# Optimization experiments

Measured on AMD Instinct MI355X. Metric: run time of the kernel, lower is better.

Reference implementation:

```python
import jax, jax.numpy as jnp
import numpy as np
import math

B, S, D, E, H = 8, 384, 768, 768, 12
HD = E // H
MAXL = 512

def _xavier(key, shape):
    fan_in, fan_out = shape[1], shape[0]
    lim = math.sqrt(6.0 / (fan_in + fan_out))
    return jax.random.uniform(key, shape, jnp.float32, -lim, lim)

def setup_inputs() -> dict:
    key = jax.random.key(0)
    ks = jax.random.split(key, 12)
    return {
        "x": jax.random.normal(ks[0], (B, S, D), jnp.float32),
        "mask": jnp.ones((B, S), jnp.int32),
        "segment_ids": jax.random.randint(ks[1], (B, S), 0, 2).astype(jnp.int32),
        "sep_distances": jax.random.normal(ks[2], (B, S), jnp.float32),
        "Wq": _xavier(ks[3], (E, D)), "bq": jnp.zeros((E,), jnp.float32),
        "Wk": _xavier(ks[4], (E, D)), "bk": jnp.zeros((E,), jnp.float32),
        "Wv": _xavier(ks[5], (E, D)), "bv": jnp.zeros((E,), jnp.float32),
        "rel_emb": jax.random.normal(ks[6], (2 * MAXL - 1, D), jnp.float32),
        "Wpk": _xavier(ks[7], (E, D)), "bpk": jnp.zeros((E,), jnp.float32),
        "Wpq": _xavier(ks[8], (E, D)), "bpq": jnp.zeros((E,), jnp.float32),
        "same_bias": jnp.zeros((H,), jnp.float32),
        "cross_bias": jnp.zeros((H,), jnp.float32),
        "sep_scale": jnp.full((H,), 0.25, jnp.float32),
        "sep_decay": jnp.full((H,), 0.35, jnp.float32),
        "Wo": _xavier(ks[9], (D, E)), "bo": jnp.zeros((D,), jnp.float32),
    }

def reference(x, mask, segment_ids, sep_distances, Wq, bq, Wk, bk, Wv, bv,
              rel_emb, Wpk, bpk, Wpq, bpq, same_bias, cross_bias,
              sep_scale, sep_decay, Wo, bo):
    b, s, _ = x.shape
    def shape_heads(t):  # [b,s,E] -> [b,H,s,HD]
        return t.reshape(b, s, H, HD).transpose(0, 2, 1, 3)
    q = shape_heads(x @ Wq.T + bq)
    k = shape_heads(x @ Wk.T + bk)
    v = shape_heads(x @ Wv.T + bv)
    # relative positions i - j, clamped and shifted
    rel_pos = jnp.arange(s)[:, None] - jnp.arange(s)[None, :]
    rel_pos = jnp.clip(rel_pos, -(MAXL - 1), MAXL - 1) + (MAXL - 1)
    rel = rel_emb[rel_pos]                     # [s,s,D]
    pos_k = (rel @ Wpk.T + bpk).reshape(s, s, H, HD)  # [i,j,h,d]
    pos_q = (rel @ Wpq.T + bpq).reshape(s, s, H, HD)
    c2c = jnp.einsum('bhid,bhjd->bhij', q, k)
    c2p = jnp.einsum('bhid,ijhd->bhij', q, pos_k)
    p2c = jnp.einsum('ijhd,bhjd->bhij', pos_q, k)
    logits = (c2c + c2p + p2c) / math.sqrt(HD * 3.0)
    # segment bias
    same = (segment_ids[:, :, None] == segment_ids[:, None, :]).astype(jnp.float32)[:, None]  # [b,1,s,s]
    cross = 1.0 - same
    hb = lambda p: p[None, :, None, None]
    seg_bias = same * hb(same_bias) + cross * hb(cross_bias)
    abs_sep = jnp.abs(sep_distances)
    gap = jnp.abs(abs_sep[:, :, None] - abs_sep[:, None, :])[:, None]  # [b,1,s,s]
    decay = jax.nn.softplus(sep_decay)[None, :, None, None] + 1e-4
    seg_bias = seg_bias + cross * jnp.exp(-gap * decay) * hb(sep_scale)
    logits = logits + seg_bias
    # mask: [b,s] -> [b,1,1,s]
    m = mask[:, None, None, :]
    logits = jnp.where(m == 0, jnp.float32(-9e15), logits)
    attn = jax.nn.softmax(logits, axis=-1)
    vals = jnp.einsum('bhij,bhjd->bhid', attn, v)
    vals = vals.transpose(0, 2, 1, 3).reshape(b, s, E)
    return vals @ Wo.T + bo
```

## Files before the change

kernel.cpp:

```cpp
#include <hip/hip_runtime.h>
#include <math.h>

#define B_  8
#define S_  384
#define H_  12
#define HD_ 64
#define E_  768
#define D_  768

typedef float  floatx4 __attribute__((ext_vector_type(4)));
typedef __bf16 bf16x8  __attribute__((ext_vector_type(8)));
typedef unsigned int ux4 __attribute__((ext_vector_type(4)));

__device__ __forceinline__ unsigned short f2bf(float f) {
    union { float f; unsigned u; } x; x.f = f;
    unsigned r = x.u + 0x7fff + ((x.u >> 16) & 1);
    return (unsigned short)(r >> 16);
}
__device__ __forceinline__ float bf2f(unsigned short u) {
    union { unsigned u; float f; } x; x.u = ((unsigned)u) << 16;
    return x.f;
}
__device__ __forceinline__ bf16x8 gld8(const unsigned short* p) {
    return __builtin_bit_cast(bf16x8, *(const ux4*)p);
}
__device__ __forceinline__ int tadr(int row, int cD) {
    return (row * 8 + (cD ^ (row & 7))) * 8;
}
__device__ __forceinline__ bf16x8 lds8(const unsigned short* base, int row, int cD) {
    return __builtin_bit_cast(bf16x8, *(const ux4*)(base + tadr(row, cD)));
}

__global__ __launch_bounds__(256) void convert_all(
    const float* __restrict__ x,
    const float* __restrict__ Wq, const float* __restrict__ Wk,
    const float* __restrict__ Wv, const float* __restrict__ Wo,
    const float* __restrict__ Wpk, const float* __restrict__ Wpq,
    const float* __restrict__ rel128,
    unsigned short* __restrict__ xb,
    unsigned short* __restrict__ wqb, unsigned short* __restrict__ wkb,
    unsigned short* __restrict__ wvb, unsigned short* __restrict__ wob,
    unsigned short* __restrict__ wpkb, unsigned short* __restrict__ wpqb,
    unsigned short* __restrict__ relb)
{
    const int seg = blockIdx.y;
    const int e = (blockIdx.x * 256 + threadIdx.x) * 4;
    const float* src;
    unsigned short* dst;
    if (seg < 4)       { src = x + (size_t)seg * 589824; dst = xb + (size_t)seg * 589824; }
    else if (seg == 4) { src = Wq;  dst = wqb; }
    else if (seg == 5) { src = Wk;  dst = wkb; }
    else if (seg == 6) { src = Wv;  dst = wvb; }
    else if (seg == 7) { src = Wo;  dst = wob; }
    else if (seg == 8) { src = Wpk; dst = wpkb; }
    else if (seg == 9) { src = Wpq; dst = wpqb; }
    else               { src = rel128; dst = relb; }

    float4 v;
    if (seg == 10 && e >= 767 * 768) v = make_float4(0.f, 0.f, 0.f, 0.f);
    else                             v = *(const float4*)(src + e);
    ushort4 o;
    o.x = f2bf(v.x); o.y = f2bf(v.y); o.z = f2bf(v.z); o.w = f2bf(v.w);
    *(ushort4*)(dst + e) = o;
}

__global__ __launch_bounds__(256) void proj_all(
    const unsigned short* __restrict__ xb, const unsigned short* __restrict__ relb,
    const unsigned short* __restrict__ wq, const unsigned short* __restrict__ wk,
    const unsigned short* __restrict__ wv, const unsigned short* __restrict__ wpk,
    const unsigned short* __restrict__ wpq,
    const float* __restrict__ bq, const float* __restrict__ bk,
    const float* __restrict__ bv, const float* __restrict__ bpk,
    const float* __restrict__ bpq,
    unsigned short* __restrict__ qb, unsigned short* __restrict__ kb,
    unsigned short* __restrict__ vtb, unsigned short* __restrict__ pkb,
    unsigned short* __restrict__ pqb)
{
    const int bid = blockIdx.x;
    int z, mt, nt;
    if (bid < 864) {
        z = bid / 288; const int r = bid - z * 288; mt = r / 6; nt = r - mt * 6;
    } else {
        const int r2 = bid - 864; z = 3 + r2 / 72;
        const int r = r2 % 72; mt = r / 6; nt = r - mt * 6;
    }
    const int m0 = mt * 64, n0 = nt * 128;

    const unsigned short* A = (z < 3) ? xb : relb;
    const unsigned short* W = (z == 0) ? wq : (z == 1) ? wk : (z == 2) ? wv
                            : (z == 3) ? wpk : wpq;
    const float* bias = (z == 0) ? bq : (z == 1) ? bk : (z == 2) ? bv
                      : (z == 3) ? bpk : bpq;
    unsigned short* C = (z == 0) ? qb : (z == 1) ? kb : (z == 2) ? vtb
                      : (z == 3) ? pkb : pqb;

    __shared__ unsigned short As[64 * 64];
    __shared__ unsigned short Ws[128 * 64];

    const int tid  = threadIdx.x;
    const int lane = tid & 63;
    const int wv_  = tid >> 6;
    const int quad = lane >> 4, l16 = lane & 15;

    floatx4 acc[4][2];
#pragma unroll
    for (int i = 0; i < 4; ++i)
#pragma unroll
        for (int j = 0; j < 2; ++j) acc[i][j] = (floatx4){0.f, 0.f, 0.f, 0.f};

    for (int k0 = 0; k0 < 768; k0 += 64) {
        __syncthreads();
#pragma unroll
        for (int r = 0; r < 2; ++r) {
            const int idx = tid + 256 * r;
            const int row = idx >> 3, cL = idx & 7, cD = cL ^ (row & 7);
            __builtin_amdgcn_global_load_lds(
                (__attribute__((address_space(1))) void*)(A + (size_t)(m0 + row) * 768 + k0 + cD * 8),
                (__attribute__((address_space(3))) void*)&As[idx * 8], 16, 0, 0);
        }
#pragma unroll
        for (int r = 0; r < 4; ++r) {
            const int idx = tid + 256 * r;
            const int row = idx >> 3, cL = idx & 7, cD = cL ^ (row & 7);
            __builtin_amdgcn_global_load_lds(
                (__attribute__((address_space(1))) void*)(W + (size_t)(n0 + row) * 768 + k0 + cD * 8),
                (__attribute__((address_space(3))) void*)&Ws[idx * 8], 16, 0, 0);
        }
        __syncthreads();

        bf16x8 a[4][2], b[2][2];
#pragma unroll
        for (int mi = 0; mi < 4; ++mi)
#pragma unroll
            for (int kc = 0; kc < 2; ++kc)
                a[mi][kc] = lds8(As, mi * 16 + l16, kc * 4 + quad);
#pragma unroll
        for (int ni = 0; ni < 2; ++ni)
#pragma unroll
            for (int kc = 0; kc < 2; ++kc)
                b[ni][kc] = lds8(Ws, wv_ * 32 + ni * 16 + l16, kc * 4 + quad);
#pragma unroll
        for (int mi = 0; mi < 4; ++mi)
#pragma unroll
            for (int ni = 0; ni < 2; ++ni)
#pragma unroll
                for (int kc = 0; kc < 2; ++kc)
                    acc[mi][ni] = __builtin_amdgcn_mfma_f32_16x16x32_bf16(
                        a[mi][kc], b[ni][kc], acc[mi][ni], 0, 0, 0);
    }

#pragma unroll
    for (int ni = 0; ni < 2; ++ni) {
        const int n = n0 + wv_ * 32 + ni * 16 + l16;
        const float bn = bias[n];
#pragma unroll
        for (int mi = 0; mi < 4; ++mi) {
            const int mbase = m0 + mi * 16 + quad * 4;
            if (z == 2) {
                const int bb = mbase / S_, s = mbase - bb * S_;
                const int h = n >> 6, hd = n & 63;
                ushort4 o;
                o.x = f2bf(acc[mi][ni][0] + bn);
                o.y = f2bf(acc[mi][ni][1] + bn);
                o.z = f2bf(acc[mi][ni][2] + bn);
                o.w = f2bf(acc[mi][ni][3] + bn);
                *(ushort4*)&C[(((size_t)(bb * H_ + h) << 6) + hd) * S_ + s] = o;
            } else if (z < 2) {
#pragma unroll
                for (int reg = 0; reg < 4; ++reg) {
                    const int m = mbase + reg;
                    const int bb = m / S_, s = m - bb * S_;
                    const int h = n >> 6, hd = n & 63;
                    C[(((size_t)(bb * H_ + h) * S_ + s) << 6) + hd] =
                        f2bf(acc[mi][ni][reg] + bn);
                }
            } else {
#pragma unroll
                for (int reg = 0; reg < 4; ++reg)
                    C[(size_t)(mbase + reg) * 768 + n] = f2bf(acc[mi][ni][reg] + bn);
            }
        }
    }
}

__global__ __launch_bounds__(256) void gemm_out(
    const unsigned short* __restrict__ A, const unsigned short* __restrict__ W,
    const float* __restrict__ bias, float* __restrict__ C)
{
    const int mt = blockIdx.x / 6, nt = blockIdx.x - mt * 6;
    const int m0 = mt * 64, n0 = nt * 128;

    __shared__ unsigned short As[64 * 64];
    __shared__ unsigned short Ws[128 * 64];

    const int tid  = threadIdx.x;
    const int lane = tid & 63;
    const int wv_  = tid >> 6;
    const int quad = lane >> 4, l16 = lane & 15;

    floatx4 acc[4][2];
#pragma unroll
    for (int i = 0; i < 4; ++i)
#pragma unroll
        for (int j = 0; j < 2; ++j) acc[i][j] = (floatx4){0.f, 0.f, 0.f, 0.f};

    for (int k0 = 0; k0 < 768; k0 += 64) {
        __syncthreads();
#pragma unroll
        for (int r = 0; r < 2; ++r) {
            const int idx = tid + 256 * r;
            const int row = idx >> 3, cL = idx & 7, cD = cL ^ (row & 7);
            __builtin_amdgcn_global_load_lds(
                (__attribute__((address_space(1))) void*)(A + (size_t)(m0 + row) * 768 + k0 + cD * 8),
                (__attribute__((address_space(3))) void*)&As[idx * 8], 16, 0, 0);
        }
#pragma unroll
        for (int r = 0; r < 4; ++r) {
            const int idx = tid + 256 * r;
            const int row = idx >> 3, cL = idx & 7, cD = cL ^ (row & 7);
            __builtin_amdgcn_global_load_lds(
                (__attribute__((address_space(1))) void*)(W + (size_t)(n0 + row) * 768 + k0 + cD * 8),
                (__attribute__((address_space(3))) void*)&Ws[idx * 8], 16, 0, 0);
        }
        __syncthreads();

        bf16x8 a[4][2], b[2][2];
#pragma unroll
        for (int mi = 0; mi < 4; ++mi)
#pragma unroll
            for (int kc = 0; kc < 2; ++kc)
                a[mi][kc] = lds8(As, mi * 16 + l16, kc * 4 + quad);
#pragma unroll
        for (int ni = 0; ni < 2; ++ni)
#pragma unroll
            for (int kc = 0; kc < 2; ++kc)
                b[ni][kc] = lds8(Ws, wv_ * 32 + ni * 16 + l16, kc * 4 + quad);
#pragma unroll
        for (int mi = 0; mi < 4; ++mi)
#pragma unroll
            for (int ni = 0; ni < 2; ++ni)
#pragma unroll
                for (int kc = 0; kc < 2; ++kc)
                    acc[mi][ni] = __builtin_amdgcn_mfma_f32_16x16x32_bf16(
                        a[mi][kc], b[ni][kc], acc[mi][ni], 0, 0, 0);
    }

#pragma unroll
    for (int ni = 0; ni < 2; ++ni) {
        const int n = n0 + wv_ * 32 + ni * 16 + l16;
        const float bn = bias[n];
#pragma unroll
        for (int mi = 0; mi < 4; ++mi)
#pragma unroll
            for (int reg = 0; reg < 4; ++reg) {
                const int m = m0 + mi * 16 + quad * 4 + reg;
                C[(size_t)m * 768 + n] = acc[mi][ni][reg] + bn;
            }
    }
}

__global__ __launch_bounds__(256, 4) void attn_mfma(
    const unsigned short* __restrict__ qg, const unsigned short* __restrict__ kg,
    const unsigned short* __restrict__ vtg,
    const unsigned short* __restrict__ pkg, const unsigned short* __restrict__ pqg,
    const int* __restrict__ seg, const float* __restrict__ sep,
    const int* __restrict__ mask,
    const float* __restrict__ same_bias, const float* __restrict__ cross_bias,
    const float* __restrict__ sep_scale, const float* __restrict__ sep_decay,
    unsigned short* __restrict__ part_O, float* __restrict__ part_ml)
{
    __shared__ float CP[64 * 68];

    const int tid  = threadIdx.x;
    const int lane = tid & 63, w = tid >> 6;
    const int l16  = lane & 15, quad = lane >> 4;
    const int ty = tid >> 4, tx = tid & 15;
    const int it = blockIdx.x, h = blockIdx.y;
    const int b  = blockIdx.z / 6, jt = blockIdx.z - 6 * b;
    const int i0 = it * 64, j0 = jt * 64;
    const size_t bh = (size_t)(b * H_ + h);

    const unsigned short* kbase  = kg  + bh * S_ * 64;
    const unsigned short* vtbase = vtg + bh * 64 * S_;
    const int dbase = i0 - j0 + 320;

    bf16x8 qf[2];
#pragma unroll
    for (int ks = 0; ks < 2; ++ks)
        qf[ks] = gld8(qg + (bh * S_ + i0 + 16 * w + l16) * 64 + ks * 32 + quad * 8);

    bf16x8 kf[4][2];
#pragma unroll
    for (int nj = 0; nj < 4; ++nj)
#pragma unroll
        for (int ks = 0; ks < 2; ++ks)
            kf[nj][ks] = gld8(kbase + (size_t)(j0 + 16 * nj + l16) * 64
                              + ks * 32 + quad * 8);

    float ai_r[4]; int si_r[4];
#pragma unroll
    for (int p = 0; p < 4; ++p) {
        const int ii = 4 * ty + p;
        ai_r[p] = fabsf(sep[b * S_ + i0 + ii]);
        si_r[p] = seg[b * S_ + i0 + ii];
    }
    float aj_r[4]; int sj_r[4], mk_r[4];
#pragma unroll
    for (int r = 0; r < 4; ++r) {
        const int jl = 4 * tx + r;
        aj_r[r] = fabsf(sep[b * S_ + j0 + jl]);
        sj_r[r] = seg[b * S_ + j0 + jl];
        mk_r[r] = mask[b * S_ + j0 + jl];
    }

    const float sb  = same_bias[h];
    const float cb  = cross_bias[h];
    const float ssc = sep_scale[h];
    const float sd  = sep_decay[h];
    const float dec = fmaxf(sd, 0.f) + log1pf(__expf(-fabsf(sd))) + 1e-4f;
    const float isc = 0.07216878364870323f;

#pragma unroll
    for (int nj = 0; nj < 4; ++nj) {
        floatx4 acc = (floatx4){0.f, 0.f, 0.f, 0.f};
#pragma unroll
        for (int ks = 0; ks < 2; ++ks)
            acc = __builtin_amdgcn_mfma_f32_16x16x32_bf16(qf[ks], kf[nj][ks], acc, 0, 0, 0);
#pragma unroll
        for (int reg = 0; reg < 4; ++reg) {
            const int ii = 16 * w + quad * 4 + reg;
            CP[ii * 68 + 16 * nj + l16] = acc[reg];
        }
    }

#pragma unroll
    for (int f = 0; f < 5; ++f) {
        const int nd = w + f;
        floatx4 acc = (floatx4){0.f, 0.f, 0.f, 0.f};
#pragma unroll
        for (int ks = 0; ks < 2; ++ks) {
            bf16x8 bf = gld8(pkg + (size_t)(dbase + 16 * nd + l16) * 768
                             + h * 64 + ks * 32 + quad * 8);
            acc = __builtin_amdgcn_mfma_f32_16x16x32_bf16(qf[ks], bf, acc, 0, 0, 0);
        }
        const int ddloc = 16 * nd + l16;
#pragma unroll
        for (int reg = 0; reg < 4; ++reg) {
            const int ii = 16 * w + quad * 4 + reg;
            const int jj = ii - ddloc + 63;
            if (jj >= 0 && jj < 64)
                CP[ii * 68 + jj] += acc[reg];
        }
    }

#pragma unroll
    for (int f = 0; f < 5; ++f) {
        const int nd = w + f;
        bf16x8 pqf[2];
#pragma unroll
        for (int ks = 0; ks < 2; ++ks)
            pqf[ks] = gld8(pqg + (size_t)(dbase + 16 * nd + l16) * 768
                           + h * 64 + ks * 32 + quad * 8);
#pragma unroll
        for (int g = 0; g < 2; ++g) {
            const int nj = (g == 0) ? (3 - f) : (4 - f);
            if (nj < 0 || nj > 3) continue;
            floatx4 acc = (floatx4){0.f, 0.f, 0.f, 0.f};
#pragma unroll
            for (int ks = 0; ks < 2; ++ks)
                acc = __builtin_amdgcn_mfma_f32_16x16x32_bf16(pqf[ks], kf[nj][ks], acc, 0, 0, 0);
            const int jj = 16 * nj + l16;
#pragma unroll
            for (int reg = 0; reg < 4; ++reg) {
                const int ddloc = 16 * nd + quad * 4 + reg;
                const int ii = ddloc + jj - 63;
                if (ii >= 16 * w && ii < 16 * w + 16)
                    CP[ii * 68 + jj] += acc[reg];
            }
        }
    }

    unsigned short* Pp = (unsigned short*)CP;
    float* pml = part_ml + (size_t)(jt * 576 + ((b * H_ + h) * 6 + it)) * 128;
#pragma unroll
    for (int p = 0; p < 4; ++p) {
        const int ii = 4 * ty + p;
        const float aii = ai_r[p];
        const int   sii = si_r[p];
        float lg[4];
        float tmax = -INFINITY;
#pragma unroll
        for (int r = 0; r < 4; ++r) {
            const int jl = 4 * tx + r;
            float xv = CP[ii * 68 + jl] * isc;
            const float gap = fabsf(aii - aj_r[r]);
            const float bias = (sii == sj_r[r]) ? sb
                             : cb + __expf(-gap * dec) * ssc;
            xv += bias;
            if (mk_r[r] == 0) xv = -9.0e15f;
            lg[r] = xv;
            tmax = fmaxf(tmax, xv);
        }
#pragma unroll
        for (int off = 1; off < 16; off <<= 1)
            tmax = fmaxf(tmax, __shfl_xor(tmax, off));
        float rs = 0.f;
        ushort4 pw;
#pragma unroll
        for (int r = 0; r < 4; ++r) {
            const float e = __expf(lg[r] - tmax);
            rs += e;
            ((unsigned short*)&pw)[r] = f2bf(e);
        }
#pragma unroll
        for (int off = 1; off < 16; off <<= 1)
            rs += __shfl_xor(rs, off);
        if (tx == 0) {
            pml[ii]      = tmax;
            pml[64 + ii] = rs;
        }
        *(ushort4*)&Pp[ii * 136 + 4 * tx] = pw;
    }

    bf16x8 pA[2];
#pragma unroll
    for (int ks = 0; ks < 2; ++ks)
        pA[ks] = __builtin_bit_cast(bf16x8,
            *(const ux4*)&Pp[(16 * w + l16) * 136 + ks * 32 + quad * 8]);
    floatx4 O[4];
#pragma unroll
    for (int nd = 0; nd < 4; ++nd) {
        O[nd] = (floatx4){0.f, 0.f, 0.f, 0.f};
#pragma unroll
        for (int ks = 0; ks < 2; ++ks) {
            bf16x8 bf = gld8(vtbase + (size_t)(16 * nd + l16) * S_
                             + j0 + ks * 32 + quad * 8);
            O[nd] = __builtin_amdgcn_mfma_f32_16x16x32_bf16(pA[ks], bf, O[nd], 0, 0, 0);
        }
    }

    unsigned short* pO = part_O + (size_t)(jt * 576 + ((b * H_ + h) * 6 + it)) * 4096;
#pragma unroll
    for (int nd = 0; nd < 4; ++nd) {
        const int d = 16 * nd + l16;
#pragma unroll
        for (int reg = 0; reg < 4; ++reg) {
            const int ii = 16 * w + quad * 4 + reg;
            pO[ii * 64 + d] = f2bf(O[nd][reg]);
        }
    }
}

__global__ __launch_bounds__(256) void merge_attn(
    const unsigned short* __restrict__ part_O, const float* __restrict__ part_ml,
    unsigned short* __restrict__ vals)
{
    const int idx = blockIdx.x;
    const int b  = idx / (H_ * 6);
    const int r  = idx - b * H_ * 6;
    const int h  = r / 6, it = r - h * 6;
    const int tid = threadIdx.x;
    const int ii = tid >> 2, c = (tid & 3) * 16;

    float m[6], l[6];
#pragma unroll
    for (int jc = 0; jc < 6; ++jc) {
        const float* pml = part_ml + (size_t)(jc * 576 + idx) * 128;
        m[jc] = pml[ii];
        l[jc] = pml[64 + ii];
    }
    float M = m[0];
#pragma unroll
    for (int jc = 1; jc < 6; ++jc) M = fmaxf(M, m[jc]);
    float wsum = 0.f, wc[6];
#pragma unroll
    for (int jc = 0; jc < 6; ++jc) {
        wc[jc] = __expf(m[jc] - M);
        wsum += wc[jc] * l[jc];
    }
    const float inv = (wsum > 0.f) ? 1.f / wsum : 0.f;

    float o[16];
#pragma unroll
    for (int e = 0; e < 16; ++e) o[e] = 0.f;
#pragma unroll
    for (int jc = 0; jc < 6; ++jc) {
        const unsigned short* pO = part_O + ((size_t)(jc * 576 + idx)) * 4096
                                 + ii * 64 + c;
        ux4 u0 = *(const ux4*)pO;
        ux4 u1 = *(const ux4*)(pO + 8);
        const unsigned short* us0 = (const unsigned short*)&u0;
        const unsigned short* us1 = (const unsigned short*)&u1;
#pragma unroll
        for (int e = 0; e < 8; ++e) {
            o[e]     += wc[jc] * bf2f(us0[e]);
            o[8 + e] += wc[jc] * bf2f(us1[e]);
        }
    }
    ushort4 w0, w1, w2, w3;
#pragma unroll
    for (int e = 0; e < 4; ++e) {
        ((unsigned short*)&w0)[e] = f2bf(o[e] * inv);
        ((unsigned short*)&w1)[e] = f2bf(o[4 + e] * inv);
        ((unsigned short*)&w2)[e] = f2bf(o[8 + e] * inv);
        ((unsigned short*)&w3)[e] = f2bf(o[12 + e] * inv);
    }
    unsigned short* dst = vals + ((size_t)(b * S_ + it * 64 + ii)) * E_ + h * 64 + c;
    *(ushort4*)(dst)      = w0;
    *(ushort4*)(dst + 4)  = w1;
    *(ushort4*)(dst + 8)  = w2;
    *(ushort4*)(dst + 12) = w3;
}

extern "C" void kernel_launch(void* const* d_in, const int* in_sizes, int n_in,
                              void* d_out, int out_size, void* d_ws, size_t ws_size,
                              hipStream_t stream)
{
    const float* x         = (const float*)d_in[0];
    const int*   mask      = (const int*)d_in[1];
    const int*   seg       = (const int*)d_in[2];
    const float* sep       = (const float*)d_in[3];
    const float* Wq        = (const float*)d_in[4];
    const float* bq        = (const float*)d_in[5];
    const float* Wk        = (const float*)d_in[6];
    const float* bk        = (const float*)d_in[7];
    const float* Wv        = (const float*)d_in[8];
    const float* bv        = (const float*)d_in[9];
    const float* rel_emb   = (const float*)d_in[10];
    const float* Wpk       = (const float*)d_in[11];
    const float* bpk       = (const float*)d_in[12];
    const float* Wpq       = (const float*)d_in[13];
    const float* bpq       = (const float*)d_in[14];
    const float* same_bias = (const float*)d_in[15];
    const float* cross_bias= (const float*)d_in[16];
    const float* sep_scale = (const float*)d_in[17];
    const float* sep_decay = (const float*)d_in[18];
    const float* Wo        = (const float*)d_in[19];
    const float* bo        = (const float*)d_in[20];

    const size_t QKVN = (size_t)B_ * S_ * E_;
    const size_t WN   = (size_t)768 * 768;

    unsigned short* xb    = (unsigned short*)d_ws;
    unsigned short* wqb   = xb   + QKVN;
    unsigned short* wkb   = wqb  + WN;
    unsigned short* wvb   = wkb  + WN;
    unsigned short* wob   = wvb  + WN;
    unsigned short* wpkb  = wob  + WN;
    unsigned short* wpqb  = wpkb + WN;
    unsigned short* relb  = wpqb + WN;
    unsigned short* qb    = relb + WN;
    unsigned short* kb    = qb   + QKVN;
    unsigned short* vtb   = kb   + QKVN;
    unsigned short* pkb   = vtb  + QKVN;
    unsigned short* pqb   = pkb  + WN;
    unsigned short* valsb = pqb  + WN;
    unsigned short* partO = valsb + QKVN;
    float*          partml= (float*)(partO + (size_t)6 * 576 * 4096);

    convert_all<<<dim3(576, 11), 256, 0, stream>>>(
        x, Wq, Wk, Wv, Wo, Wpk, Wpq, rel_emb + (size_t)128 * D_,
        xb, wqb, wkb, wvb, wob, wpkb, wpqb, relb);

    proj_all<<<dim3(1008), 256, 0, stream>>>(
        xb, relb, wqb, wkb, wvb, wpkb, wpqb,
        bq, bk, bv, bpk, bpq, qb, kb, vtb, pkb, pqb);

    attn_mfma<<<dim3(6, 12, 48), 256, 0, stream>>>(
        qb, kb, vtb, pkb, pqb, seg, sep, mask,
        same_bias, cross_bias, sep_scale, sep_decay, partO, partml);

    merge_attn<<<dim3(576), 256, 0, stream>>>(partO, partml, valsb);

    gemm_out<<<dim3(288), 256, 0, stream>>>(valsb, wob, bo, (float*)d_out);
}
```

Measured before the change: 218.6 us.

## Cut attention split-K from six j-chunks to two with online softmax

Each attention block now loops over three 64-wide key tiles with a running max and sum (online softmax), instead of handling a single key tile. This cuts the number of partial outputs per query tile from six to two, and the merge kernel now combines only two partials. The aim is to reduce partial-result write and read traffic and merge work. In exchange the grid is one third the size, there is more serial work per block, and the occupancy hint drops from 4 to 3 blocks per CU, which may hurt latency hiding.

```diff
diff --git a/kernel.cpp b/kernel.cpp
--- a/kernel.cpp
+++ b/kernel.cpp
@@ -259,7 +259,7 @@
     }
 }
 
-__global__ __launch_bounds__(256, 4) void attn_mfma(
+__global__ __launch_bounds__(256, 3) void attn_mfma(
     const unsigned short* __restrict__ qg, const unsigned short* __restrict__ kg,
     const unsigned short* __restrict__ vtg,
     const unsigned short* __restrict__ pkg, const unsigned short* __restrict__ pqg,
@@ -276,26 +276,17 @@
     const int l16  = lane & 15, quad = lane >> 4;
     const int ty = tid >> 4, tx = tid & 15;
     const int it = blockIdx.x, h = blockIdx.y;
-    const int b  = blockIdx.z / 6, jt = blockIdx.z - 6 * b;
-    const int i0 = it * 64, j0 = jt * 64;
+    const int b  = blockIdx.z >> 1, jh = blockIdx.z & 1;
+    const int i0 = it * 64;
     const size_t bh = (size_t)(b * H_ + h);
 
     const unsigned short* kbase  = kg  + bh * S_ * 64;
     const unsigned short* vtbase = vtg + bh * 64 * S_;
-    const int dbase = i0 - j0 + 320;
 
     bf16x8 qf[2];
 #pragma unroll
     for (int ks = 0; ks < 2; ++ks)
         qf[ks] = gld8(qg + (bh * S_ + i0 + 16 * w + l16) * 64 + ks * 32 + quad * 8);
-
-    bf16x8 kf[4][2];
-#pragma unroll
-    for (int nj = 0; nj < 4; ++nj)
-#pragma unroll
-        for (int ks = 0; ks < 2; ++ks)
-            kf[nj][ks] = gld8(kbase + (size_t)(j0 + 16 * nj + l16) * 64
-                              + ks * 32 + quad * 8);
 
     float ai_r[4]; int si_r[4];
 #pragma unroll
@@ -303,14 +294,6 @@
         const int ii = 4 * ty + p;
         ai_r[p] = fabsf(sep[b * S_ + i0 + ii]);
         si_r[p] = seg[b * S_ + i0 + ii];
-    }
-    float aj_r[4]; int sj_r[4], mk_r[4];
-#pragma unroll
-    for (int r = 0; r < 4; ++r) {
-        const int jl = 4 * tx + r;
-        aj_r[r] = fabsf(sep[b * S_ + j0 + jl]);
-        sj_r[r] = seg[b * S_ + j0 + jl];
-        mk_r[r] = mask[b * S_ + j0 + jl];
     }
 
     const float sb  = same_bias[h];
@@ -320,126 +303,163 @@
     const float dec = fmaxf(sd, 0.f) + log1pf(__expf(-fabsf(sd))) + 1e-4f;
     const float isc = 0.07216878364870323f;
 
-#pragma unroll
-    for (int nj = 0; nj < 4; ++nj) {
-        floatx4 acc = (floatx4){0.f, 0.f, 0.f, 0.f};
-#pragma unroll
-        for (int ks = 0; ks < 2; ++ks)
-            acc = __builtin_amdgcn_mfma_f32_16x16x32_bf16(qf[ks], kf[nj][ks], acc, 0, 0, 0);
-#pragma unroll
-        for (int reg = 0; reg < 4; ++reg) {
-            const int ii = 16 * w + quad * 4 + reg;
-            CP[ii * 68 + 16 * nj + l16] = acc[reg];
-        }
-    }
-
-#pragma unroll
-    for (int f = 0; f < 5; ++f) {
-        const int nd = w + f;
-        floatx4 acc = (floatx4){0.f, 0.f, 0.f, 0.f};
-#pragma unroll
-        for (int ks = 0; ks < 2; ++ks) {
-            bf16x8 bf = gld8(pkg + (size_t)(dbase + 16 * nd + l16) * 768
-                             + h * 64 + ks * 32 + quad * 8);
-            acc = __builtin_amdgcn_mfma_f32_16x16x32_bf16(qf[ks], bf, acc, 0, 0, 0);
-        }
-        const int ddloc = 16 * nd + l16;
-#pragma unroll
-        for (int reg = 0; reg < 4; ++reg) {
-            const int ii = 16 * w + quad * 4 + reg;
-            const int jj = ii - ddloc + 63;
-            if (jj >= 0 && jj < 64)
-                CP[ii * 68 + jj] += acc[reg];
-        }
-    }
-
-#pragma unroll
-    for (int f = 0; f < 5; ++f) {
-        const int nd = w + f;
-        bf16x8 pqf[2];
-#pragma unroll
-        for (int ks = 0; ks < 2; ++ks)
-            pqf[ks] = gld8(pqg + (size_t)(dbase + 16 * nd + l16) * 768
-                           + h * 64 + ks * 32 + quad * 8);
-#pragma unroll
-        for (int g = 0; g < 2; ++g) {
-            const int nj = (g == 0) ? (3 - f) : (4 - f);
-            if (nj < 0 || nj > 3) continue;
-            floatx4 acc = (floatx4){0.f, 0.f, 0.f, 0.f};
-#pragma unroll
-            for (int ks = 0; ks < 2; ++ks)
-                acc = __builtin_amdgcn_mfma_f32_16x16x32_bf16(pqf[ks], kf[nj][ks], acc, 0, 0, 0);
-            const int jj = 16 * nj + l16;
-#pragma unroll
-            for (int reg = 0; reg < 4; ++reg) {
-                const int ddloc = 16 * nd + quad * 4 + reg;
-                const int ii = ddloc + jj - 63;
-                if (ii >= 16 * w && ii < 16 * w + 16)
-                    CP[ii * 68 + jj] += acc[reg];
-            }
-        }
-    }
+    float m_run[4], l_run[4];
+#pragma unroll
+    for (int p = 0; p < 4; ++p) { m_run[p] = -INFINITY; l_run[p] = 0.f; }
+    floatx4 O[4];
+#pragma unroll
+    for (int nd = 0; nd < 4; ++nd) O[nd] = (floatx4){0.f, 0.f, 0.f, 0.f};
 
     unsigned short* Pp = (unsigned short*)CP;
-    float* pml = part_ml + (size_t)(jt * 576 + ((b * H_ + h) * 6 + it)) * 128;
-#pragma unroll
-    for (int p = 0; p < 4; ++p) {
-        const int ii = 4 * ty + p;
-        const float aii = ai_r[p];
-        const int   sii = si_r[p];
-        float lg[4];
-        float tmax = -INFINITY;
+
+#pragma unroll
+    for (int t = 0; t < 3; ++t) {
+        const int j0 = jh * 192 + t * 64;
+        const int dbase = i0 - j0 + 320;
+
+        float aj_r[4]; int sj_r[4], mk_r[4];
 #pragma unroll
         for (int r = 0; r < 4; ++r) {
             const int jl = 4 * tx + r;
-            float xv = CP[ii * 68 + jl] * isc;
-            const float gap = fabsf(aii - aj_r[r]);
-            const float bias = (sii == sj_r[r]) ? sb
-                             : cb + __expf(-gap * dec) * ssc;
-            xv += bias;
-            if (mk_r[r] == 0) xv = -9.0e15f;
-            lg[r] = xv;
-            tmax = fmaxf(tmax, xv);
-        }
-#pragma unroll
-        for (int off = 1; off < 16; off <<= 1)
-            tmax = fmaxf(tmax, __shfl_xor(tmax, off));
-        float rs = 0.f;
-        ushort4 pw;
-#pragma unroll
-        for (int r = 0; r < 4; ++r) {
-            const float e = __expf(lg[r] - tmax);
-            rs += e;
-            ((unsigned short*)&pw)[r] = f2bf(e);
-        }
-#pragma unroll
-        for (int off = 1; off < 16; off <<= 1)
-            rs += __shfl_xor(rs, off);
-        if (tx == 0) {
-            pml[ii]      = tmax;
-            pml[64 + ii] = rs;
-        }
-        *(ushort4*)&Pp[ii * 136 + 4 * tx] = pw;
-    }
-
-    bf16x8 pA[2];
-#pragma unroll
-    for (int ks = 0; ks < 2; ++ks)
-        pA[ks] = __builtin_bit_cast(bf16x8,
-            *(const ux4*)&Pp[(16 * w + l16) * 136 + ks * 32 + quad * 8]);
-    floatx4 O[4];
-#pragma unroll
-    for (int nd = 0; nd < 4; ++nd) {
-        O[nd] = (floatx4){0.f, 0.f, 0.f, 0.f};
-#pragma unroll
-        for (int ks = 0; ks < 2; ++ks) {
-            bf16x8 bf = gld8(vtbase + (size_t)(16 * nd + l16) * S_
-                             + j0 + ks * 32 + quad * 8);
-            O[nd] = __builtin_amdgcn_mfma_f32_16x16x32_bf16(pA[ks], bf, O[nd], 0, 0, 0);
-        }
-    }
-
-    unsigned short* pO = part_O + (size_t)(jt * 576 + ((b * H_ + h) * 6 + it)) * 4096;
+            aj_r[r] = fabsf(sep[b * S_ + j0 + jl]);
+            sj_r[r] = seg[b * S_ + j0 + jl];
+            mk_r[r] = mask[b * S_ + j0 + jl];
+        }
+
+        bf16x8 kf[4][2];
+#pragma unroll
+        for (int nj = 0; nj < 4; ++nj)
+#pragma unroll
+            for (int ks = 0; ks < 2; ++ks)
+                kf[nj][ks] = gld8(kbase + (size_t)(j0 + 16 * nj + l16) * 64
+                                  + ks * 32 + quad * 8);
+
+#pragma unroll
+        for (int nj = 0; nj < 4; ++nj) {
+            floatx4 acc = (floatx4){0.f, 0.f, 0.f, 0.f};
+#pragma unroll
+            for (int ks = 0; ks < 2; ++ks)
+                acc = __builtin_amdgcn_mfma_f32_16x16x32_bf16(qf[ks], kf[nj][ks], acc, 0, 0, 0);
+#pragma unroll
+            for (int reg = 0; reg < 4; ++reg) {
+                const int ii = 16 * w + quad * 4 + reg;
+                CP[ii * 68 + 16 * nj + l16] = acc[reg];
+            }
+        }
+
+#pragma unroll
+        for (int f = 0; f < 5; ++f) {
+            const int nd = w + f;
+            floatx4 acc = (floatx4){0.f, 0.f, 0.f, 0.f};
+#pragma unroll
+            for (int ks = 0; ks < 2; ++ks) {
+                bf16x8 bf = gld8(pkg + (size_t)(dbase + 16 * nd + l16) * 768
+                                 + h * 64 + ks * 32 + quad * 8);
+                acc = __builtin_amdgcn_mfma_f32_16x16x32_bf16(qf[ks], bf, acc, 0, 0, 0);
+            }
+            const int ddloc = 16 * nd + l16;
+#pragma unroll
+            for (int reg = 0; reg < 4; ++reg) {
+                const int ii = 16 * w + quad * 4 + reg;
+                const int jj = ii - ddloc + 63;
+                if (jj >= 0 && jj < 64)
+                    CP[ii * 68 + jj] += acc[reg];
+            }
+        }
+
+#pragma unroll
+        for (int f = 0; f < 5; ++f) {
+            const int nd = w + f;
+            bf16x8 pqf[2];
+#pragma unroll
+            for (int ks = 0; ks < 2; ++ks)
+                pqf[ks] = gld8(pqg + (size_t)(dbase + 16 * nd + l16) * 768
+                               + h * 64 + ks * 32 + quad * 8);
+#pragma unroll
+            for (int g = 0; g < 2; ++g) {
+                const int nj = (g == 0) ? (3 - f) : (4 - f);
+                if (nj < 0 || nj > 3) continue;
+                floatx4 acc = (floatx4){0.f, 0.f, 0.f, 0.f};
+#pragma unroll
+                for (int ks = 0; ks < 2; ++ks)
+                    acc = __builtin_amdgcn_mfma_f32_16x16x32_bf16(pqf[ks], kf[nj][ks], acc, 0, 0, 0);
+                const int jj = 16 * nj + l16;
+#pragma unroll
+                for (int reg = 0; reg < 4; ++reg) {
+                    const int ddloc = 16 * nd + quad * 4 + reg;
+                    const int ii = ddloc + jj - 63;
+                    if (ii >= 16 * w && ii < 16 * w + 16)
+                        CP[ii * 68 + jj] += acc[reg];
+                }
+            }
+        }
+
+        float sc_arr[4];
+#pragma unroll
+        for (int p = 0; p < 4; ++p) {
+            const int ii = 4 * ty + p;
+            const float aii = ai_r[p];
+            const int   sii = si_r[p];
+            float lg[4];
+            float tmax = -INFINITY;
+#pragma unroll
+            for (int r = 0; r < 4; ++r) {
+                const int jl = 4 * tx + r;
+                float xv = CP[ii * 68 + jl] * isc;
+                const float gap = fabsf(aii - aj_r[r]);
+                const float bias = (sii == sj_r[r]) ? sb
+                                 : cb + __expf(-gap * dec) * ssc;
+                xv += bias;
+                if (mk_r[r] == 0) xv = -9.0e15f;
+                lg[r] = xv;
+                tmax = fmaxf(tmax, xv);
+            }
+#pragma unroll
+            for (int off = 1; off < 16; off <<= 1)
+                tmax = fmaxf(tmax, __shfl_xor(tmax, off));
+            const float newm = fmaxf(m_run[p], tmax);
+            const float scale = __expf(m_run[p] - newm);
+            m_run[p] = newm;
+            sc_arr[p] = scale;
+            float rs = 0.f;
+            ushort4 pw;
+#pragma unroll
+            for (int r = 0; r < 4; ++r) {
+                const float e = __expf(lg[r] - newm);
+                rs += e;
+                ((unsigned short*)&pw)[r] = f2bf(e);
+            }
+#pragma unroll
+            for (int off = 1; off < 16; off <<= 1)
+                rs += __shfl_xor(rs, off);
+            l_run[p] = l_run[p] * scale + rs;
+            *(ushort4*)&Pp[ii * 136 + 4 * tx] = pw;
+        }
+
+#pragma unroll
+        for (int nd = 0; nd < 4; ++nd)
+#pragma unroll
+            for (int reg = 0; reg < 4; ++reg)
+                O[nd][reg] *= sc_arr[reg];
+
+        bf16x8 pA[2];
+#pragma unroll
+        for (int ks = 0; ks < 2; ++ks)
+            pA[ks] = __builtin_bit_cast(bf16x8,
+                *(const ux4*)&Pp[(16 * w + l16) * 136 + ks * 32 + quad * 8]);
+#pragma unroll
+        for (int nd = 0; nd < 4; ++nd) {
+#pragma unroll
+            for (int ks = 0; ks < 2; ++ks) {
+                bf16x8 bf = gld8(vtbase + (size_t)(16 * nd + l16) * S_
+                                 + j0 + ks * 32 + quad * 8);
+                O[nd] = __builtin_amdgcn_mfma_f32_16x16x32_bf16(pA[ks], bf, O[nd], 0, 0, 0);
+            }
+        }
+    }
+
+    const int idx = (int)((b * H_ + h) * 6 + it);
+    unsigned short* pO = part_O + (size_t)(jh * 576 + idx) * 4096;
 #pragma unroll
     for (int nd = 0; nd < 4; ++nd) {
         const int d = 16 * nd + l16;
@@ -447,6 +467,15 @@
         for (int reg = 0; reg < 4; ++reg) {
             const int ii = 16 * w + quad * 4 + reg;
             pO[ii * 64 + d] = f2bf(O[nd][reg]);
+        }
+    }
+    float* pml = part_ml + (size_t)(jh * 576 + idx) * 128;
+    if (tx == 0) {
+#pragma unroll
+        for (int p = 0; p < 4; ++p) {
+            const int ii = 4 * ty + p;
+            pml[ii]      = m_run[p];
+            pml[64 + ii] = l_run[p];
         }
     }
 }
@@ -462,19 +491,17 @@
     const int tid = threadIdx.x;
     const int ii = tid >> 2, c = (tid & 3) * 16;
 
-    float m[6], l[6];
-#pragma unroll
-    for (int jc = 0; jc < 6; ++jc) {
+    float m[2], l[2];
+#pragma unroll
+    for (int jc = 0; jc < 2; ++jc) {
         const float* pml = part_ml + (size_t)(jc * 576 + idx) * 128;
         m[jc] = pml[ii];
         l[jc] = pml[64 + ii];
     }
-    float M = m[0];
-#pragma unroll
-    for (int jc = 1; jc < 6; ++jc) M = fmaxf(M, m[jc]);
-    float wsum = 0.f, wc[6];
-#pragma unroll
-    for (int jc = 0; jc < 6; ++jc) {
+    float M = fmaxf(m[0], m[1]);
+    float wsum = 0.f, wc[2];
+#pragma unroll
+    for (int jc = 0; jc < 2; ++jc) {
         wc[jc] = __expf(m[jc] - M);
         wsum += wc[jc] * l[jc];
     }
@@ -484,7 +511,7 @@
 #pragma unroll
     for (int e = 0; e < 16; ++e) o[e] = 0.f;
 #pragma unroll
-    for (int jc = 0; jc < 6; ++jc) {
+    for (int jc = 0; jc < 2; ++jc) {
         const unsigned short* pO = part_O + ((size_t)(jc * 576 + idx)) * 4096
                                  + ii * 64 + c;
         ux4 u0 = *(const ux4*)pO;
@@ -556,7 +583,7 @@
     unsigned short* pqb   = pkb  + WN;
     unsigned short* valsb = pqb  + WN;
     unsigned short* partO = valsb + QKVN;
-    float*          partml= (float*)(partO + (size_t)6 * 576 * 4096);
+    float*          partml= (float*)(partO + (size_t)2 * 576 * 4096);
 
     convert_all<<<dim3(576, 11), 256, 0, stream>>>(
         x, Wq, Wk, Wv, Wo, Wpk, Wpq, rel_emb + (size_t)128 * D_,
@@ -566,7 +593,7 @@
         xb, relb, wqb, wkb, wvb, wpkb, wpqb,
         bq, bk, bv, bpk, bpq, qb, kb, vtb, pkb, pqb);
 
-    attn_mfma<<<dim3(6, 12, 48), 256, 0, stream>>>(
+    attn_mfma<<<dim3(6, 12, 16), 256, 0, stream>>>(
         qb, kb, vtb, pkb, pqb, seg, sep, mask,
         same_bias, cross_bias, sep_scale, sep_decay, partO, partml);
 
```

Measured after the change: 220.5 us. No clear change (+0.9%).

## Compute softmax in MFMA A-fragment layout and feed P from registers

Applied to the files above, without the earlier changes.

Each lane now handles one query row and the 16 key columns that match its MFMA A-operand fragment, instead of a 16x16 thread tiling over rows. The softmax probabilities are packed to bf16 in registers and used directly as the A operand for the P·V MFMA. This drops the LDS write/read round trip of P and shortens the shuffle reductions. Per-column sep/seg/mask values are loaded with vector loads. Occupancy bound is lowered from 4 to 3 blocks per CU to give room for the extra registers. Whether the removed LDS traffic and the cheaper reductions outweigh the higher register use and lower occupancy is not certain.

```diff
diff --git a/kernel.cpp b/kernel.cpp
--- a/kernel.cpp
+++ b/kernel.cpp
@@ -259,7 +259,7 @@
     }
 }
 
-__global__ __launch_bounds__(256, 4) void attn_mfma(
+__global__ __launch_bounds__(256, 3) void attn_mfma(
     const unsigned short* __restrict__ qg, const unsigned short* __restrict__ kg,
     const unsigned short* __restrict__ vtg,
     const unsigned short* __restrict__ pkg, const unsigned short* __restrict__ pqg,
@@ -274,7 +274,6 @@
     const int tid  = threadIdx.x;
     const int lane = tid & 63, w = tid >> 6;
     const int l16  = lane & 15, quad = lane >> 4;
-    const int ty = tid >> 4, tx = tid & 15;
     const int it = blockIdx.x, h = blockIdx.y;
     const int b  = blockIdx.z / 6, jt = blockIdx.z - 6 * b;
     const int i0 = it * 64, j0 = jt * 64;
@@ -297,21 +296,25 @@
             kf[nj][ks] = gld8(kbase + (size_t)(j0 + 16 * nj + l16) * 64
                               + ks * 32 + quad * 8);
 
-    float ai_r[4]; int si_r[4];
-#pragma unroll
-    for (int p = 0; p < 4; ++p) {
-        const int ii = 4 * ty + p;
-        ai_r[p] = fabsf(sep[b * S_ + i0 + ii]);
-        si_r[p] = seg[b * S_ + i0 + ii];
-    }
-    float aj_r[4]; int sj_r[4], mk_r[4];
-#pragma unroll
-    for (int r = 0; r < 4; ++r) {
-        const int jl = 4 * tx + r;
-        aj_r[r] = fabsf(sep[b * S_ + j0 + jl]);
-        sj_r[r] = seg[b * S_ + j0 + jl];
-        mk_r[r] = mask[b * S_ + j0 + jl];
-    }
+    const int row = 16 * w + l16;
+    const float aii = fabsf(sep[b * S_ + i0 + row]);
+    const int   sii = seg[b * S_ + i0 + row];
+    const float* sepj = sep  + b * S_ + j0;
+    const int*   segj = seg  + b * S_ + j0;
+    const int*   mskj = mask + b * S_ + j0;
+    float ajv[16]; int sjv[16], mkv[16];
+    *(float4*)&ajv[0]  = *(const float4*)&sepj[quad * 8];
+    *(float4*)&ajv[4]  = *(const float4*)&sepj[quad * 8 + 4];
+    *(float4*)&ajv[8]  = *(const float4*)&sepj[32 + quad * 8];
+    *(float4*)&ajv[12] = *(const float4*)&sepj[32 + quad * 8 + 4];
+    *(int4*)&sjv[0]  = *(const int4*)&segj[quad * 8];
+    *(int4*)&sjv[4]  = *(const int4*)&segj[quad * 8 + 4];
+    *(int4*)&sjv[8]  = *(const int4*)&segj[32 + quad * 8];
+    *(int4*)&sjv[12] = *(const int4*)&segj[32 + quad * 8 + 4];
+    *(int4*)&mkv[0]  = *(const int4*)&mskj[quad * 8];
+    *(int4*)&mkv[4]  = *(const int4*)&mskj[quad * 8 + 4];
+    *(int4*)&mkv[8]  = *(const int4*)&mskj[32 + quad * 8];
+    *(int4*)&mkv[12] = *(const int4*)&mskj[32 + quad * 8 + 4];
 
     const float sb  = same_bias[h];
     const float cb  = cross_bias[h];
@@ -380,53 +383,50 @@
         }
     }
 
-    unsigned short* Pp = (unsigned short*)CP;
+    floatx4 cp0 = *(const floatx4*)&CP[row * 68 + quad * 8];
+    floatx4 cp1 = *(const floatx4*)&CP[row * 68 + quad * 8 + 4];
+    floatx4 cp2 = *(const floatx4*)&CP[row * 68 + 32 + quad * 8];
+    floatx4 cp3 = *(const floatx4*)&CP[row * 68 + 32 + quad * 8 + 4];
+
+    float lg[16];
+    float tmax = -INFINITY;
+#pragma unroll
+    for (int e = 0; e < 16; ++e) {
+        const float cpv = (e < 4) ? cp0[e] : (e < 8) ? cp1[e - 4]
+                        : (e < 12) ? cp2[e - 8] : cp3[e - 12];
+        float xv = cpv * isc;
+        const float gap = fabsf(aii - fabsf(ajv[e]));
+        const float bias = (sii == sjv[e]) ? sb
+                         : cb + __expf(-gap * dec) * ssc;
+        xv += bias;
+        if (mkv[e] == 0) xv = -9.0e15f;
+        lg[e] = xv;
+        tmax = fmaxf(tmax, xv);
+    }
+    tmax = fmaxf(tmax, __shfl_xor(tmax, 16));
+    tmax = fmaxf(tmax, __shfl_xor(tmax, 32));
+
+    float rs = 0.f;
+    unsigned int pk32[8];
+#pragma unroll
+    for (int e = 0; e < 8; ++e) {
+        const float e0 = __expf(lg[2 * e]     - tmax);
+        const float e1 = __expf(lg[2 * e + 1] - tmax);
+        rs += e0 + e1;
+        pk32[e] = (unsigned)f2bf(e0) | ((unsigned)f2bf(e1) << 16);
+    }
+    rs += __shfl_xor(rs, 16);
+    rs += __shfl_xor(rs, 32);
+
     float* pml = part_ml + (size_t)(jt * 576 + ((b * H_ + h) * 6 + it)) * 128;
-#pragma unroll
-    for (int p = 0; p < 4; ++p) {
-        const int ii = 4 * ty + p;
-        const float aii = ai_r[p];
-        const int   sii = si_r[p];
-        float lg[4];
-        float tmax = -INFINITY;
-#pragma unroll
-        for (int r = 0; r < 4; ++r) {
-            const int jl = 4 * tx + r;
-            float xv = CP[ii * 68 + jl] * isc;
-            const float gap = fabsf(aii - aj_r[r]);
-            const float bias = (sii == sj_r[r]) ? sb
-                             : cb + __expf(-gap * dec) * ssc;
-            xv += bias;
-            if (mk_r[r] == 0) xv = -9.0e15f;
-            lg[r] = xv;
-            tmax = fmaxf(tmax, xv);
-        }
-#pragma unroll
-        for (int off = 1; off < 16; off <<= 1)
-            tmax = fmaxf(tmax, __shfl_xor(tmax, off));
-        float rs = 0.f;
-        ushort4 pw;
-#pragma unroll
-        for (int r = 0; r < 4; ++r) {
-            const float e = __expf(lg[r] - tmax);
-            rs += e;
-            ((unsigned short*)&pw)[r] = f2bf(e);
-        }
-#pragma unroll
-        for (int off = 1; off < 16; off <<= 1)
-            rs += __shfl_xor(rs, off);
-        if (tx == 0) {
-            pml[ii]      = tmax;
-            pml[64 + ii] = rs;
-        }
-        *(ushort4*)&Pp[ii * 136 + 4 * tx] = pw;
+    if (quad == 0) {
+        pml[row]      = tmax;
+        pml[64 + row] = rs;
     }
 
     bf16x8 pA[2];
-#pragma unroll
-    for (int ks = 0; ks < 2; ++ks)
-        pA[ks] = __builtin_bit_cast(bf16x8,
-            *(const ux4*)&Pp[(16 * w + l16) * 136 + ks * 32 + quad * 8]);
+    pA[0] = __builtin_bit_cast(bf16x8, (ux4){pk32[0], pk32[1], pk32[2], pk32[3]});
+    pA[1] = __builtin_bit_cast(bf16x8, (ux4){pk32[4], pk32[5], pk32[6], pk32[7]});
     floatx4 O[4];
 #pragma unroll
     for (int nd = 0; nd < 4; ++nd) {
```

New measurement: 220.3 us. About the same (+0.8%).
